# Kernel optimization log

Measured on AMD Instinct MI355X. Metric: run time of the kernel, lower is better.

The kernel has to match this reference:

```python
import jax, jax.numpy as jnp
import numpy as np

DIM = 2048
H = 16
QLR = 1536
KVLR = 512
NOPE = 128
ROPE = 64
VH = 128
QKH = NOPE + ROPE  # 192
B, S = 2, 2048
EPS = 1e-6


def _rmsnorm(x, w):
    return x * jax.lax.rsqrt(jnp.mean(x * x, axis=-1, keepdims=True) + EPS) * w


def _rope_cos_sin(seq_len, r, dtype):
    inv_freq = 1.0 / (10000.0 ** (jnp.arange(0, r, 2, dtype=jnp.float32) / r))
    ang = jnp.arange(seq_len, dtype=jnp.float32)[:, None] * inv_freq  # [S, r/2]
    return jnp.cos(ang).astype(dtype), jnp.sin(ang).astype(dtype)


def _rot(t, cos, sin):
    # rotate-half RoPE on last dim; cos/sin pre-broadcast to t's rank
    t1, t2 = jnp.split(t, 2, axis=-1)
    return jnp.concatenate([t1 * cos - t2 * sin, t2 * cos + t1 * sin], axis=-1)


def setup_inputs() -> dict:
    key = jax.random.key(0)
    ks = jax.random.split(key, 12)
    sd = 0.02
    return {
        "x": jax.random.normal(ks[0], (B, S, DIM), jnp.float32),
        "wqd": jax.random.normal(ks[1], (DIM, QLR), jnp.float32) * sd,
        "bqd": jnp.zeros((QLR,), jnp.float32),
        "qnorm_w": jnp.ones((QLR,), jnp.float32),
        "wqu": jax.random.normal(ks[2], (QLR, H * QKH), jnp.float32) * sd,
        "bqu": jnp.zeros((H * QKH,), jnp.float32),
        "wkvd": jax.random.normal(ks[3], (DIM, KVLR + ROPE), jnp.float32) * sd,
        "bkvd": jnp.zeros((KVLR + ROPE,), jnp.float32),
        "kvnorm_w": jnp.ones((KVLR,), jnp.float32),
        "wkvu": jax.random.normal(ks[4], (KVLR, H * (NOPE + VH)), jnp.float32) * sd,
        "bkvu": jnp.zeros((H * (NOPE + VH),), jnp.float32),
        "wout": jax.random.normal(ks[5], (H * VH, DIM), jnp.float32) * sd,
        "bout": jnp.zeros((DIM,), jnp.float32),
    }


def reference(x, wqd, bqd, qnorm_w, wqu, bqu, wkvd, bkvd, kvnorm_w, wkvu, bkvu, wout, bout):
    b, s, _ = x.shape
    # Q path: low-rank down, RMSNorm, up; split nope / rope
    q = _rmsnorm(x @ wqd + bqd, qnorm_w) @ wqu + bqu        # [b,s,H*QKH]
    q = q.reshape(b, s, H, QKH)
    q_nope, q_rope = q[..., :NOPE], q[..., NOPE:]
    # KV path: joint down-proj -> kv latent + shared rope key
    kvd = x @ wkvd + bkvd                                   # [b,s,KVLR+ROPE]
    kv_lora, k_rope = kvd[..., :KVLR], kvd[..., KVLR:]
    cos, sin = _rope_cos_sin(s, ROPE, x.dtype)
    q_rope = _rot(q_rope, cos[None, :, None, :], sin[None, :, None, :])
    k_rope = _rot(k_rope, cos[None, :, :], sin[None, :, :])  # [b,s,ROPE]
    kvu = _rmsnorm(kv_lora, kvnorm_w) @ wkvu + bkvu          # [b,s,H*(NOPE+VH)]
    kvu = kvu.reshape(b, s, H, NOPE + VH)
    k_nope, v = kvu[..., :NOPE], kvu[..., NOPE:]
    k_rope_b = jnp.broadcast_to(k_rope[:, :, None, :], (b, s, H, ROPE))
    qf = jnp.concatenate([q_nope, q_rope], axis=-1)          # [b,s,H,QKH]
    kf = jnp.concatenate([k_nope, k_rope_b], axis=-1)        # [b,s,H,QKH]
    scale = QKH ** -0.5
    scores = jnp.einsum('bqhd,bkhd->bhqk', qf, kf) * scale
    causal = jnp.tril(jnp.ones((s, s), bool))
    scores = jnp.where(causal, scores, jnp.finfo(scores.dtype).min)
    attn = jax.nn.softmax(scores, axis=-1)
    o = jnp.einsum('bhqk,bkhd->bqhd', attn, v).reshape(b, s, H * VH)
    return o @ wout + bout
```

## Files before the change

### kernel.cpp

```cpp
#include <hip/hip_runtime.h>
#include <hip/hip_bf16.h>
#include <math.h>

#define HH 16
#define SS 2048
#define BBATCH 2
#define NROWS 4096

typedef __attribute__((ext_vector_type(8))) __bf16 bf16x8;
typedef __attribute__((ext_vector_type(4))) float f32x4;
typedef const __attribute__((address_space(1))) unsigned int* gas1_t;
typedef __attribute__((address_space(3))) unsigned int* las3_t;

__device__ __forceinline__ unsigned short f2bf(float f) {
  unsigned u = __builtin_bit_cast(unsigned, f);
  u += 0x7fffu + ((u >> 16) & 1u);
  return (unsigned short)(u >> 16);
}
__device__ __forceinline__ float bf2f(unsigned short u) {
  return __builtin_bit_cast(float, (unsigned)u << 16);
}

__device__ __forceinline__ void gload16(const void* g, void* l) {
  __builtin_amdgcn_global_load_lds((gas1_t)g, (las3_t)l, 16, 0, 0);
}
__device__ __forceinline__ f32x4 mfma16(bf16x8 a, bf16x8 b, f32x4 c) {
  return __builtin_amdgcn_mfma_f32_16x16x32_bf16(a, b, c, 0, 0, 0);
}

__device__ __forceinline__ void transpose_body(const float* __restrict__ W,
                                               unsigned short* __restrict__ Wt,
                                               int K, int N, int Npad,
                                               int bx, int by, float (*tile)[33], int tid) {
  int n0 = bx * 32, k0 = by * 32;
  int tx = tid & 31, ty = tid >> 5;
  for (int i = ty; i < 32; i += 8) {
    int k = k0 + i, n = n0 + tx;
    tile[i][tx] = (k < K && n < N) ? W[(long)k * N + n] : 0.f;
  }
  __syncthreads();
  for (int i = ty; i < 32; i += 8) {
    int n = n0 + i, k = k0 + tx;
    if (n < Npad && k < K) Wt[(long)n * K + k] = f2bf(tile[tx][i]);
  }
}

__global__ __launch_bounds__(256) void k_prep(const float* __restrict__ x,
                                              unsigned short* __restrict__ xb,
                                              const float* __restrict__ wqd,
                                              const float* __restrict__ wqu,
                                              const float* __restrict__ wkvd,
                                              const float* __restrict__ wkvu,
                                              const float* __restrict__ wout,
                                              unsigned short* __restrict__ wqkt,
                                              unsigned short* __restrict__ wqut,
                                              unsigned short* __restrict__ wkvut,
                                              unsigned short* __restrict__ woutt,
                                              const float* __restrict__ bqd,
                                              const float* __restrict__ bkvd,
                                              float* __restrict__ mbias,
                                              float2* __restrict__ rtab) {
  __shared__ float tile[32][33];
  int blk = blockIdx.x;
  int tid = threadIdx.x;
  if (blk < 2048) {
    long n4 = (long)NROWS * 2048 / 4;
    for (long i = (long)blk * 256 + tid; i < n4; i += 2048 * 256) {
      float4 v = ((const float4*)x)[i];
      ushort4 o = { f2bf(v.x), f2bf(v.y), f2bf(v.z), f2bf(v.w) };
      ((ushort4*)xb)[i] = o;
    }
  } else if (blk < 5120) {
    int t = blk - 2048;
    transpose_body(wqd, wqkt, 2048, 1536, 1536, t % 48, t / 48, tile, tid);
  } else if (blk < 9728) {
    int t = blk - 5120;
    transpose_body(wqu, wqut, 1536, 3072, 3072, t % 96, t / 96, tile, tid);
  } else if (blk < 11008) {
    int t = blk - 9728;
    transpose_body(wkvd, wqkt + (size_t)1536 * 2048, 2048, 576, 640, t % 20, t / 20, tile, tid);
  } else if (blk < 13056) {
    int t = blk - 11008;
    transpose_body(wkvu, wkvut, 512, 4096, 4096, t % 128, t / 128, tile, tid);
  } else if (blk < 17152) {
    int t = blk - 13056;
    transpose_body(wout, woutt, 2048, 2048, 2048, t % 64, t / 64, tile, tid);
  } else if (blk < 17161) {
    int i = (blk - 17152) * 256 + tid;
    if (i < 2176) mbias[i] = i < 1536 ? bqd[i] : (i < 2112 ? bkvd[i - 1536] : 0.f);
  } else {
    int t = blk - 17161;
    int s = t * 8 + (tid >> 5);
    int i = tid & 31;
    float inv = powf(10000.f, -(float)i / 32.f);
    float ang = (float)s * inv;
    float sn, cs;
    sincosf(ang, &sn, &cs);
    rtab[s * 32 + i] = make_float2(cs, sn);
  }
}

__global__ __launch_bounds__(256) void k_gemm(const unsigned short* __restrict__ A,
                                              const unsigned short* __restrict__ Bt,
                                              const float* __restrict__ bias,
                                              float* __restrict__ C,
                                              int M, int N, int K) {
  __shared__ unsigned short lA[128 * 32];
  __shared__ unsigned short lB[128 * 32];
  int tid = threadIdx.x;
  int wave = tid >> 6, lane = tid & 63;
  int l15 = lane & 15, lhi = lane >> 4;
  int ntn = (N + 127) >> 7;
  int tm = blockIdx.x / ntn, tn = blockIdx.x % ntn;
  long row0 = (long)tm * 128, col0 = (long)tn * 128;
  int wr = wave >> 1, wc = wave & 1;

  const unsigned short* gA = A + (row0 + (tid >> 2)) * K + (tid & 3) * 8;
  const unsigned short* gB = Bt + (col0 + (tid >> 2)) * K + (tid & 3) * 8;
  unsigned short* lA0 = &lA[tid * 8];
  unsigned short* lB0 = &lB[tid * 8];

  f32x4 acc[4][4] = {};
  for (int k0 = 0; k0 < K; k0 += 32) {
    __syncthreads();
    gload16(gA + k0, lA0);
    gload16(gA + (long)64 * K + k0, lA0 + 2048);
    gload16(gB + k0, lB0);
    gload16(gB + (long)64 * K + k0, lB0 + 2048);
    asm volatile("s_waitcnt vmcnt(0)" ::: "memory");
    __syncthreads();
    bf16x8 af[4], bfr[4];
#pragma unroll
    for (int i = 0; i < 4; ++i) {
      af[i]  = *(const bf16x8*)&lA[(wr * 64 + i * 16 + l15) * 32 + lhi * 8];
      bfr[i] = *(const bf16x8*)&lB[(wc * 64 + i * 16 + l15) * 32 + lhi * 8];
    }
#pragma unroll
    for (int i = 0; i < 4; ++i)
#pragma unroll
      for (int j = 0; j < 4; ++j)
        acc[i][j] = mfma16(af[i], bfr[j], acc[i][j]);
  }
#pragma unroll
  for (int i = 0; i < 4; ++i)
#pragma unroll
    for (int j = 0; j < 4; ++j) {
      long r = row0 + wr * 64 + i * 16 + lhi * 4;
      long c = col0 + wc * 64 + j * 16 + l15;
      if (c < N) {
        float bv = bias[c];
#pragma unroll
        for (int rr = 0; rr < 4; ++rr)
          C[(r + rr) * N + c] = acc[i][j][rr] + bv;
      }
    }
}

__global__ __launch_bounds__(256) void k_gemm_c16(const unsigned short* __restrict__ A,
                                                  const unsigned short* __restrict__ Bt,
                                                  const float* __restrict__ bias,
                                                  unsigned short* __restrict__ C,
                                                  int M, int N, int K) {
  __shared__ unsigned short lA[128 * 32];
  __shared__ unsigned short lB[128 * 32];
  int tid = threadIdx.x;
  int wave = tid >> 6, lane = tid & 63;
  int l15 = lane & 15, lhi = lane >> 4;
  int ntn = (N + 127) >> 7;
  int tm = blockIdx.x / ntn, tn = blockIdx.x % ntn;
  long row0 = (long)tm * 128, col0 = (long)tn * 128;
  int wr = wave >> 1, wc = wave & 1;

  const unsigned short* gA = A + (row0 + (tid >> 2)) * K + (tid & 3) * 8;
  const unsigned short* gB = Bt + (col0 + (tid >> 2)) * K + (tid & 3) * 8;
  unsigned short* lA0 = &lA[tid * 8];
  unsigned short* lB0 = &lB[tid * 8];

  f32x4 acc[4][4] = {};
  for (int k0 = 0; k0 < K; k0 += 32) {
    __syncthreads();
    gload16(gA + k0, lA0);
    gload16(gA + (long)64 * K + k0, lA0 + 2048);
    gload16(gB + k0, lB0);
    gload16(gB + (long)64 * K + k0, lB0 + 2048);
    asm volatile("s_waitcnt vmcnt(0)" ::: "memory");
    __syncthreads();
    bf16x8 af[4], bfr[4];
#pragma unroll
    for (int i = 0; i < 4; ++i) {
      af[i]  = *(const bf16x8*)&lA[(wr * 64 + i * 16 + l15) * 32 + lhi * 8];
      bfr[i] = *(const bf16x8*)&lB[(wc * 64 + i * 16 + l15) * 32 + lhi * 8];
    }
#pragma unroll
    for (int i = 0; i < 4; ++i)
#pragma unroll
      for (int j = 0; j < 4; ++j)
        acc[i][j] = mfma16(af[i], bfr[j], acc[i][j]);
  }
#pragma unroll
  for (int i = 0; i < 4; ++i)
#pragma unroll
    for (int j = 0; j < 4; ++j) {
      long r = row0 + wr * 64 + i * 16 + lhi * 4;
      long c = col0 + wc * 64 + j * 16 + l15;
      if (c < N) {
        float bv = bias[c];
#pragma unroll
        for (int rr = 0; rr < 4; ++rr)
          C[(r + rr) * N + c] = f2bf(acc[i][j][rr] + bv);
      }
    }
}

__global__ __launch_bounds__(256) void k_gemm_qf(const unsigned short* __restrict__ A,
                                                 const unsigned short* __restrict__ Bt,
                                                 const float* __restrict__ bias,
                                                 const float2* __restrict__ rtab,
                                                 unsigned short* __restrict__ qf,
                                                 int M, int N, int K) {
  __shared__ unsigned short lA[128 * 32];
  __shared__ unsigned short lB[128 * 32];
  int tid = threadIdx.x;
  int wave = tid >> 6, lane = tid & 63;
  int l15 = lane & 15, lhi = lane >> 4;
  int ntn = (N + 127) >> 7;
  int tm = blockIdx.x / ntn, tn = blockIdx.x % ntn;
  long row0 = (long)tm * 128, col0 = (long)tn * 128;
  int wr = wave >> 1, wc = wave & 1;

  const unsigned short* gA = A + (row0 + (tid >> 2)) * K + (tid & 3) * 8;
  const unsigned short* gB = Bt + (col0 + (tid >> 2)) * K + (tid & 3) * 8;
  unsigned short* lA0 = &lA[tid * 8];
  unsigned short* lB0 = &lB[tid * 8];

  f32x4 acc[4][4] = {};
  for (int k0 = 0; k0 < K; k0 += 32) {
    __syncthreads();
    gload16(gA + k0, lA0);
    gload16(gA + (long)64 * K + k0, lA0 + 2048);
    gload16(gB + k0, lB0);
    gload16(gB + (long)64 * K + k0, lB0 + 2048);
    asm volatile("s_waitcnt vmcnt(0)" ::: "memory");
    __syncthreads();
    bf16x8 af[4], bfr[4];
#pragma unroll
    for (int i = 0; i < 4; ++i) {
      af[i]  = *(const bf16x8*)&lA[(wr * 64 + i * 16 + l15) * 32 + lhi * 8];
      bfr[i] = *(const bf16x8*)&lB[(wc * 64 + i * 16 + l15) * 32 + lhi * 8];
    }
#pragma unroll
    for (int i = 0; i < 4; ++i)
#pragma unroll
      for (int j = 0; j < 4; ++j)
        acc[i][j] = mfma16(af[i], bfr[j], acc[i][j]);
  }

  const float scq = 0.07216878364870322f * 1.4426950408889634f;
  int base = (int)col0 + wc * 64;
  int h = base / 192;
  int m192 = base - h * 192;
  float bv[4];
#pragma unroll
  for (int j = 0; j < 4; ++j) bv[j] = bias[base + j * 16 + l15];

#pragma unroll
  for (int i = 0; i < 4; ++i) {
#pragma unroll
    for (int rr = 0; rr < 4; ++rr) {
      long r = row0 + wr * 64 + i * 16 + lhi * 4 + rr;
      int s = (int)(r & 2047), b = (int)(r >> 11);
      unsigned short* dst = qf + (((long)(b * HH + h)) * SS + s) * 192;
      if (m192 < 128) {
#pragma unroll
        for (int j = 0; j < 4; ++j)
          dst[m192 + j * 16 + l15] = f2bf((acc[i][j][rr] + bv[j]) * scq);
      } else {
#pragma unroll
        for (int j = 0; j < 2; ++j) {
          int ifq = j * 16 + l15;
          float2 cs = rtab[s * 32 + ifq];
          float v1 = acc[i][j][rr] + bv[j];
          float v2 = acc[i][j + 2][rr] + bv[j + 2];
          dst[128 + ifq] = f2bf((v1 * cs.x - v2 * cs.y) * scq);
          dst[160 + ifq] = f2bf((v2 * cs.x + v1 * cs.y) * scq);
        }
      }
    }
  }
}

__global__ __launch_bounds__(256) void k_gemm_kv(const unsigned short* __restrict__ A,
                                                 const unsigned short* __restrict__ Bt,
                                                 const float* __restrict__ bias,
                                                 unsigned short* __restrict__ kf3,
                                                 unsigned short* __restrict__ vt3,
                                                 int M, int N, int K) {
  __shared__ unsigned short smem[16384];
  unsigned short* lA = smem;
  unsigned short* lB = smem + 4096;
  int tid = threadIdx.x;
  int wave = tid >> 6, lane = tid & 63;
  int l15 = lane & 15, lhi = lane >> 4;
  int ntn = N >> 7;
  int tm = blockIdx.x / ntn, tn = blockIdx.x % ntn;
  long row0 = (long)tm * 128, col0 = (long)tn * 128;
  int wr = wave >> 1, wc = wave & 1;

  const unsigned short* gA = A + (row0 + (tid >> 2)) * K + (tid & 3) * 8;
  const unsigned short* gB = Bt + (col0 + (tid >> 2)) * K + (tid & 3) * 8;
  unsigned short* lA0 = &lA[tid * 8];
  unsigned short* lB0 = &lB[tid * 8];

  f32x4 acc[4][4] = {};
  for (int k0 = 0; k0 < K; k0 += 32) {
    __syncthreads();
    gload16(gA + k0, lA0);
    gload16(gA + (long)64 * K + k0, lA0 + 2048);
    gload16(gB + k0, lB0);
    gload16(gB + (long)64 * K + k0, lB0 + 2048);
    asm volatile("s_waitcnt vmcnt(0)" ::: "memory");
    __syncthreads();
    bf16x8 af[4], bfr[4];
#pragma unroll
    for (int i = 0; i < 4; ++i) {
      af[i]  = *(const bf16x8*)&lA[(wr * 64 + i * 16 + l15) * 32 + lhi * 8];
      bfr[i] = *(const bf16x8*)&lB[(wc * 64 + i * 16 + l15) * 32 + lhi * 8];
    }
#pragma unroll
    for (int i = 0; i < 4; ++i)
#pragma unroll
      for (int j = 0; j < 4; ++j)
        acc[i][j] = mfma16(af[i], bfr[j], acc[i][j]);
  }

  int base = (int)col0 + wc * 64;
  int h = base >> 8;
  bool isv = (base & 255) >= 128;
  float bv[4];
#pragma unroll
  for (int j = 0; j < 4; ++j) bv[j] = bias[base + j * 16 + l15];

  int b = (int)(row0 >> 11);
  long bh = (long)b * HH + h;
  int lrb = wr * 64;
  __syncthreads();

  if (isv) {
#pragma unroll
    for (int i = 0; i < 4; ++i) {
      int lr = lrb + i * 16 + lhi * 4;
#pragma unroll
      for (int j = 0; j < 4; ++j) {
        int lc = wc * 64 + j * 16 + l15;
        ushort4 pk = { f2bf(acc[i][j][0] + bv[j]), f2bf(acc[i][j][1] + bv[j]),
                       f2bf(acc[i][j][2] + bv[j]), f2bf(acc[i][j][3] + bv[j]) };
        *(ushort4*)&smem[((lr >> 5) << 12) + lc * 32 + (lr & 31)] = pk;
      }
    }
    __syncthreads();
    long dst0 = (bh * 64 + ((row0 & 2047) >> 5)) * 4096;
#pragma unroll
    for (int p = 0; p < 8; ++p) {
      int e = p * 256 + tid;
      *(uint4*)&vt3[dst0 + e * 8] = *(uint4*)&smem[e * 8];
    }
  } else {
#pragma unroll
    for (int i = 0; i < 4; ++i) {
      int lr0 = lrb + i * 16 + lhi * 4;
#pragma unroll
      for (int j = 0; j < 4; ++j) {
        int c = (base & 255) + j * 16 + l15;
        int tbase = ((lr0 >> 4) << 11) + ((c >> 5) << 9) + (((c >> 3) & 3) << 7) + (c & 7);
#pragma unroll
        for (int rr = 0; rr < 4; ++rr)
          smem[tbase + ((lr0 + rr) & 15) * 8] = f2bf(acc[i][j][rr] + bv[j]);
      }
    }
    __syncthreads();
    long kb3 = (bh * 128 + ((row0 & 2047) >> 4)) * 3072;
#pragma unroll
    for (int p = 0; p < 8; ++p) {
      int e = p * 256 + tid;
      int tile = e >> 6;
      int off = (e & 63) * 8;
      long dst = kb3 + ((long)(tile >> 2) * 6 + (tile & 3)) * 512 + off;
      *(uint4*)&kf3[dst] = *(uint4*)&smem[tile * 512 + off];
    }
  }
}

__global__ __launch_bounds__(256) void k_rmsnorm2(const unsigned short* __restrict__ sC,
                                                  const float* __restrict__ qnw,
                                                  const float* __restrict__ kvnw,
                                                  unsigned short* __restrict__ qn,
                                                  unsigned short* __restrict__ kvn) {
  int blk = blockIdx.x;
  long row;
  const unsigned short* x;
  const float* w;
  unsigned short* y;
  int L;
  if (blk < NROWS) {
    row = blk; x = sC + row * 2176; w = qnw; y = qn + row * 1536; L = 1536;
  } else {
    row = blk - NROWS; x = sC + row * 2176 + 1536; w = kvnw; y = kvn + row * 512; L = 512;
  }
  float ss = 0.f;
  int n4 = L >> 2;
  for (int i = threadIdx.x; i < n4; i += 256) {
    ushort4 v = ((const ushort4*)x)[i];
    float a = bf2f(v.x), bb = bf2f(v.y), c = bf2f(v.z), d = bf2f(v.w);
    ss += a * a + bb * bb + c * c + d * d;
  }
  for (int off = 32; off > 0; off >>= 1) ss += __shfl_xor(ss, off);
  __shared__ float sb[4];
  if ((threadIdx.x & 63) == 0) sb[threadIdx.x >> 6] = ss;
  __syncthreads();
  float scale = rsqrtf((sb[0] + sb[1] + sb[2] + sb[3]) / (float)L + 1e-6f);
  for (int i = threadIdx.x; i < L; i += 256)
    y[i] = f2bf(bf2f(x[i]) * scale * w[i]);
}

__global__ __launch_bounds__(64) void k_extract_krope(const unsigned short* __restrict__ sC,
                                                      const float2* __restrict__ rtab,
                                                      unsigned short* __restrict__ kf3) {
  int bs = blockIdx.x;
  int lane = threadIdx.x;
  int s = bs & (SS - 1), b = bs >> 11;
  const unsigned short* src = sC + (long)bs * 2176 + 2048;
  int i = lane & 31;
  float2 cs = rtab[s * 32 + i];
  float t1 = bf2f(src[i]), t2 = bf2f(src[32 + i]);
  float v = (lane < 32) ? (t1 * cs.x - t2 * cs.y) : (t2 * cs.x + t1 * cs.y);
  unsigned short bv = f2bf(v);
  int d = 128 + lane;
  long inner = (long)(d >> 5) * 512 + ((d >> 3) & 3) * 128 + (s & 15) * 8 + (d & 7);
#pragma unroll
  for (int h = 0; h < HH; ++h) {
    long blk = ((long)(b * HH + h) * 128 + (s >> 4)) * 6;
    kf3[blk * 512 + inner] = bv;
  }
}

__global__ __launch_bounds__(256, 4) void k_attn(const unsigned short* __restrict__ qf,
                                                 const unsigned short* __restrict__ kf3,
                                                 const unsigned short* __restrict__ vt3,
                                                 unsigned short* __restrict__ o,
                                                 float* __restrict__ pO,
                                                 float* __restrict__ pml) {
  __shared__ unsigned short kbuf[64 * 192];
  __shared__ unsigned short pbuf[4][16 * 72];
  int tid = threadIdx.x;
  int wave = tid >> 6, lane = tid & 63;
  int l15 = lane & 15, lhi = lane >> 4;
  int idx = blockIdx.x;
  int rp = idx >> 5, bh = idx & 31;
  int qt, part, np;
  if (rp < 32)      { qt = 24 + (rp >> 2); part = rp & 3; np = 4; }
  else if (rp < 56) { int r = rp - 32; qt = 16 + r / 3; part = r % 3; np = 3; }
  else if (rp < 72) { int r = rp - 56; qt = 8 + (r >> 1); part = r & 1; np = 2; }
  else              { qt = 79 - rp; part = 0; np = 1; }
  int nt = qt + 1;
  int t0 = nt * part / np, t1 = nt * (part + 1) / np;
  bool dodiag = (part == np - 1);
  int item;
  if (np == 1) item = -1;
  else {
    int base = (qt < 16) ? (qt - 8) * 2 : (qt < 24) ? 16 + (qt - 16) * 3 : 40 + (qt - 24) * 4;
    item = bh * 72 + base + part;
  }
  int b = bh >> 4, h = bh & 15;
  int q0 = qt * 64;
  const char* kbase = (const char*)(kf3 + (long)bh * 128 * 3072);
  const unsigned short* vfrag0 = vt3 + (long)bh * 64 * 4096 + l15 * 32 + lhi * 8;
  const unsigned short* kread = kbuf + lane * 8;
  unsigned psel = 0x07060302u;

  {
    const char* src = kbase + (long)t0 * 24576 + tid * 16;
    char* dst = (char*)kbuf + tid * 16;
#pragma unroll
    for (int p = 0; p < 6; ++p) gload16(src + p * 4096, dst + p * 4096);
  }

  const unsigned short* Qb = qf + ((long)bh * SS + q0 + wave * 16 + l15) * 192 + lhi * 8;
  bf16x8 qfr[6];
#pragma unroll
  for (int ks = 0; ks < 6; ++ks) qfr[ks] = *(const bf16x8*)(Qb + ks * 32);

  float m = -3e38f, ls = 0.f;
  f32x4 acc[8] = {};
  int qin = wave * 16 + l15;

  for (int t = t0; t < t1; ++t) {
    asm volatile("s_waitcnt vmcnt(0)" ::: "memory");
    __builtin_amdgcn_s_barrier();
    __builtin_amdgcn_sched_barrier(0);

    f32x4 sc[4] = {};
    __builtin_amdgcn_s_setprio(1);
#pragma unroll
    for (int ks = 0; ks < 6; ++ks) {
      bf16x8 kfr[4];
#pragma unroll
      for (int nf = 0; nf < 4; ++nf)
        kfr[nf] = *(const bf16x8*)&kread[(nf * 6 + ks) * 512];
#pragma unroll
      for (int nf = 0; nf < 4; ++nf)
        sc[nf] = mfma16(kfr[nf], qfr[ks], sc[nf]);
    }
    __builtin_amdgcn_s_setprio(0);
    __builtin_amdgcn_sched_barrier(0);
    __builtin_amdgcn_s_barrier();
    __builtin_amdgcn_sched_barrier(0);

    const unsigned short* vtb = vfrag0 + (long)t * 8192;
    bf16x8 v0[8];
#pragma unroll
    for (int nf = 0; nf < 8; ++nf) v0[nf] = *(const bf16x8*)(vtb + nf * 512);
    __builtin_amdgcn_sched_barrier(0);

    if (t + 1 < t1) {
      const char* src = kbase + (long)(t + 1) * 24576 + tid * 16;
      char* dst = (char*)kbuf + tid * 16;
#pragma unroll
      for (int p = 0; p < 6; ++p) gload16(src + p * 4096, dst + p * 4096);
    }

    bool diag = dodiag && (t == t1 - 1);
    float mnf[4];
#pragma unroll
    for (int nf = 0; nf < 4; ++nf) {
      if (diag) {
#pragma unroll
        for (int jj = 0; jj < 4; ++jj) {
          int kin = nf * 16 + lhi * 4 + jj;
          if (kin > qin) sc[nf][jj] = -3e38f;
        }
      }
      mnf[nf] = fmaxf(fmaxf(sc[nf][0], sc[nf][1]), fmaxf(sc[nf][2], sc[nf][3]));
    }
    float mx = fmaxf(fmaxf(mnf[0], mnf[1]), fmaxf(mnf[2], mnf[3]));
    mx = fmaxf(mx, __shfl_xor(mx, 16));
    mx = fmaxf(mx, __shfl_xor(mx, 32));
    if (!__all(mx <= m + 8.f)) {
      float mn = fmaxf(m, mx);
      float alpha = exp2f(m - mn);
      m = mn;
      ls *= alpha;
#pragma unroll
      for (int nf = 0; nf < 8; ++nf)
#pragma unroll
        for (int jj = 0; jj < 4; ++jj) acc[nf][jj] *= alpha;
    }
    float pnf[4];
#pragma unroll
    for (int nf = 0; nf < 4; ++nf) {
      float e0 = exp2f(sc[nf][0] - m), e1 = exp2f(sc[nf][1] - m);
      float e2 = exp2f(sc[nf][2] - m), e3 = exp2f(sc[nf][3] - m);
      pnf[nf] = (e0 + e1) + (e2 + e3);
      unsigned lo, hi;
      asm("v_perm_b32 %0, %1, %2, %3" : "=v"(lo) : "v"(e1), "v"(e0), "s"(psel));
      asm("v_perm_b32 %0, %1, %2, %3" : "=v"(hi) : "v"(e3), "v"(e2), "s"(psel));
      uint2 pk = { lo, hi };
      *(uint2*)&pbuf[wave][l15 * 72 + nf * 16 + lhi * 4] = pk;
    }
    float ps = (pnf[0] + pnf[1]) + (pnf[2] + pnf[3]);
    ps += __shfl_xor(ps, 16);
    ps += __shfl_xor(ps, 32);
    ls += ps;

    {
      bf16x8 pf = *(const bf16x8*)&pbuf[wave][l15 * 72 + lhi * 8];
      __builtin_amdgcn_s_setprio(1);
#pragma unroll
      for (int nf = 0; nf < 8; ++nf) acc[nf] = mfma16(v0[nf], pf, acc[nf]);
      __builtin_amdgcn_s_setprio(0);
    }
    bf16x8 v1[8];
#pragma unroll
    for (int nf = 0; nf < 8; ++nf) v1[nf] = *(const bf16x8*)(vtb + 4096 + nf * 512);
    {
      bf16x8 pf = *(const bf16x8*)&pbuf[wave][l15 * 72 + 32 + lhi * 8];
      __builtin_amdgcn_s_setprio(1);
#pragma unroll
      for (int nf = 0; nf < 8; ++nf) acc[nf] = mfma16(v1[nf], pf, acc[nf]);
      __builtin_amdgcn_s_setprio(0);
    }
  }

  int qloc = wave * 16 + l15;
  if (item < 0) {
    float invl = 1.f / ls;
    long orow = (long)b * SS + q0 + qloc;
#pragma unroll
    for (int nf = 0; nf < 8; ++nf) {
      ushort4 ov = { f2bf(acc[nf][0] * invl), f2bf(acc[nf][1] * invl),
                     f2bf(acc[nf][2] * invl), f2bf(acc[nf][3] * invl) };
      *(ushort4*)&o[orow * 2048 + h * 128 + nf * 16 + lhi * 4] = ov;
    }
  } else {
    float* po = pO + (long)item * 8192 + qloc * 128;
#pragma unroll
    for (int nf = 0; nf < 8; ++nf)
      *(float4*)&po[nf * 16 + lhi * 4] = __builtin_bit_cast(float4, acc[nf]);
    if (lhi == 0) {
      pml[(long)item * 128 + qloc * 2] = m;
      pml[(long)item * 128 + qloc * 2 + 1] = ls;
    }
  }
}

__global__ __launch_bounds__(256) void k_merge(const float* __restrict__ pO,
                                               const float* __restrict__ pml,
                                               unsigned short* __restrict__ o) {
  int g = blockIdx.x;
  int bh = g / 24, qt = (g % 24) + 8;
  int b = bh >> 4, h = bh & 15;
  int q0 = qt * 64;
  int np = qt < 16 ? 2 : (qt < 24 ? 3 : 4);
  int base = (qt < 16) ? (qt - 8) * 2 : (qt < 24) ? 16 + (qt - 16) * 3 : 40 + (qt - 24) * 4;
  long i0 = (long)bh * 72 + base;
  __shared__ float wts[4][64];
  int tid = threadIdx.x;
  if (tid < 64) {
    float mp0 = -3e38f, mp1 = -3e38f, mp2 = -3e38f, mp3 = -3e38f;
    float lp0 = 0.f, lp1 = 0.f, lp2 = 0.f, lp3 = 0.f;
    mp0 = pml[(i0 + 0) * 128 + tid * 2]; lp0 = pml[(i0 + 0) * 128 + tid * 2 + 1];
    mp1 = pml[(i0 + 1) * 128 + tid * 2]; lp1 = pml[(i0 + 1) * 128 + tid * 2 + 1];
    if (np > 2) { mp2 = pml[(i0 + 2) * 128 + tid * 2]; lp2 = pml[(i0 + 2) * 128 + tid * 2 + 1]; }
    if (np > 3) { mp3 = pml[(i0 + 3) * 128 + tid * 2]; lp3 = pml[(i0 + 3) * 128 + tid * 2 + 1]; }
    float mm = fmaxf(fmaxf(mp0, mp1), fmaxf(mp2, mp3));
    float w0 = exp2f(mp0 - mm), w1 = exp2f(mp1 - mm);
    float w2 = (np > 2) ? exp2f(mp2 - mm) : 0.f;
    float w3 = (np > 3) ? exp2f(mp3 - mm) : 0.f;
    float inv = 1.f / (lp0 * w0 + lp1 * w1 + lp2 * w2 + lp3 * w3);
    wts[0][tid] = w0 * inv; wts[1][tid] = w1 * inv;
    wts[2][tid] = w2 * inv; wts[3][tid] = w3 * inv;
  }
  __syncthreads();
#pragma unroll
  for (int pp = 0; pp < 8; ++pp) {
    int e = pp * 256 + tid;
    int q = e >> 5, d4 = (e & 31) * 4;
    float4 s = { 0.f, 0.f, 0.f, 0.f };
#pragma unroll
    for (int p = 0; p < 4; ++p) {
      if (p < np) {
        float4 a = *(const float4*)&pO[(i0 + p) * 8192 + q * 128 + d4];
        float w = wts[p][q];
        s.x += a.x * w; s.y += a.y * w; s.z += a.z * w; s.w += a.w * w;
      }
    }
    ushort4 ov = { f2bf(s.x), f2bf(s.y), f2bf(s.z), f2bf(s.w) };
    *(ushort4*)&o[((long)b * SS + q0 + q) * 2048 + h * 128 + d4] = ov;
  }
}

extern "C" void kernel_launch(void* const* d_in, const int* in_sizes, int n_in,
                              void* d_out, int out_size, void* d_ws, size_t ws_size,
                              hipStream_t stream) {
  const float* x    = (const float*)d_in[0];
  const float* wqd  = (const float*)d_in[1];
  const float* bqd  = (const float*)d_in[2];
  const float* qnw  = (const float*)d_in[3];
  const float* wqu  = (const float*)d_in[4];
  const float* bqu  = (const float*)d_in[5];
  const float* wkvd = (const float*)d_in[6];
  const float* bkvd = (const float*)d_in[7];
  const float* kvnw = (const float*)d_in[8];
  const float* wkvu = (const float*)d_in[9];
  const float* bkvu = (const float*)d_in[10];
  const float* wout = (const float*)d_in[11];
  const float* bout = (const float*)d_in[12];
  float* out = (float*)d_out;

  char* ws = (char*)d_ws;
  size_t off = 0;
  auto alloc = [&](size_t sz) {
    char* p = ws + off;
    off += (sz + 255) & ~(size_t)255;
    return p;
  };
  unsigned short* xb    = (unsigned short*)alloc((size_t)NROWS * 2048 * 2);
  unsigned short* wqkt  = (unsigned short*)alloc((size_t)2176 * 2048 * 2);
  unsigned short* wqut  = (unsigned short*)alloc((size_t)3072 * 1536 * 2);
  unsigned short* wkvut = (unsigned short*)alloc((size_t)4096 * 512 * 2);
  unsigned short* woutt = (unsigned short*)alloc((size_t)2048 * 2048 * 2);
  unsigned short* qn    = (unsigned short*)alloc((size_t)NROWS * 1536 * 2);
  unsigned short* kvn   = (unsigned short*)alloc((size_t)NROWS * 512 * 2);
  unsigned short* qfb   = (unsigned short*)alloc((size_t)32 * SS * 192 * 2);
  unsigned short* kfb   = (unsigned short*)alloc((size_t)32 * SS * 192 * 2);
  unsigned short* vtb   = (unsigned short*)alloc((size_t)32 * 128 * SS * 2);
  unsigned short* ob    = (unsigned short*)alloc((size_t)NROWS * 2048 * 2);
  float*  mbias = (float*)alloc((size_t)2176 * 4);
  float2* rtab  = (float2*)alloc((size_t)SS * 32 * 8);
  float*  pO    = (float*)alloc((size_t)2304 * 8192 * 4);
  float*  pml   = (float*)alloc((size_t)2304 * 128 * 4);
  unsigned short* sCb = (unsigned short*)alloc((size_t)NROWS * 2176 * 2);

  k_prep<<<17417, 256, 0, stream>>>(x, xb, wqd, wqu, wkvd, wkvu, wout,
                                    wqkt, wqut, wkvut, woutt, bqd, bkvd, mbias, rtab);

  k_gemm_c16<<<32 * 17, 256, 0, stream>>>(xb, wqkt, mbias, sCb, NROWS, 2176, 2048);

  k_rmsnorm2<<<2 * NROWS, 256, 0, stream>>>(sCb, qnw, kvnw, qn, kvn);

  k_gemm_qf<<<32 * 24, 256, 0, stream>>>(qn, wqut, bqu, rtab, qfb, NROWS, 3072, 1536);

  k_extract_krope<<<NROWS, 64, 0, stream>>>(sCb, rtab, kfb);
  k_gemm_kv<<<32 * 32, 256, 0, stream>>>(kvn, wkvut, bkvu, kfb, vtb, NROWS, 4096, 512);

  k_attn<<<2560, 256, 0, stream>>>(qfb, kfb, vtb, ob, pO, pml);
  k_merge<<<768, 256, 0, stream>>>(pO, pml, ob);

  k_gemm<<<32 * 16, 256, 0, stream>>>(ob, woutt, bout, out, NROWS, 2048, 2048);
}
```

Baseline: 400.4 us.

## Merge Q/KV up-projection and k-rope kernels into one launch; swizzle attn P buffer

```diff
diff --git a/kernel.cpp b/kernel.cpp
--- a/kernel.cpp
+++ b/kernel.cpp
@@ -212,180 +212,185 @@
     }
 }
 
-__global__ __launch_bounds__(256) void k_gemm_qf(const unsigned short* __restrict__ A,
-                                                 const unsigned short* __restrict__ Bt,
-                                                 const float* __restrict__ bias,
-                                                 const float2* __restrict__ rtab,
-                                                 unsigned short* __restrict__ qf,
-                                                 int M, int N, int K) {
-  __shared__ unsigned short lA[128 * 32];
-  __shared__ unsigned short lB[128 * 32];
+__global__ __launch_bounds__(256) void k_up(const unsigned short* __restrict__ qn,
+                                            const unsigned short* __restrict__ wqut,
+                                            const float* __restrict__ bqu,
+                                            const unsigned short* __restrict__ kvn,
+                                            const unsigned short* __restrict__ wkvut,
+                                            const float* __restrict__ bkvu,
+                                            const unsigned short* __restrict__ sCb,
+                                            const float2* __restrict__ rtab,
+                                            unsigned short* __restrict__ qf,
+                                            unsigned short* __restrict__ kf3,
+                                            unsigned short* __restrict__ vt3) {
+  __shared__ unsigned short smem[16384];
+  unsigned short* lA = smem;
+  unsigned short* lB = smem + 4096;
+  int blk = blockIdx.x;
   int tid = threadIdx.x;
   int wave = tid >> 6, lane = tid & 63;
   int l15 = lane & 15, lhi = lane >> 4;
-  int ntn = (N + 127) >> 7;
-  int tm = blockIdx.x / ntn, tn = blockIdx.x % ntn;
-  long row0 = (long)tm * 128, col0 = (long)tn * 128;
   int wr = wave >> 1, wc = wave & 1;
 
-  const unsigned short* gA = A + (row0 + (tid >> 2)) * K + (tid & 3) * 8;
-  const unsigned short* gB = Bt + (col0 + (tid >> 2)) * K + (tid & 3) * 8;
-  unsigned short* lA0 = &lA[tid * 8];
-  unsigned short* lB0 = &lB[tid * 8];
-
-  f32x4 acc[4][4] = {};
-  for (int k0 = 0; k0 < K; k0 += 32) {
+  if (blk < 768) {
+    const int N = 3072, K = 1536;
+    int tm = blk / 24, tn = blk % 24;
+    long row0 = (long)tm * 128, col0 = (long)tn * 128;
+    const unsigned short* gA = qn + (row0 + (tid >> 2)) * K + (tid & 3) * 8;
+    const unsigned short* gB = wqut + (col0 + (tid >> 2)) * K + (tid & 3) * 8;
+    unsigned short* lA0 = &lA[tid * 8];
+    unsigned short* lB0 = &lB[tid * 8];
+    f32x4 acc[4][4] = {};
+    for (int k0 = 0; k0 < K; k0 += 32) {
+      __syncthreads();
+      gload16(gA + k0, lA0);
+      gload16(gA + (long)64 * K + k0, lA0 + 2048);
+      gload16(gB + k0, lB0);
+      gload16(gB + (long)64 * K + k0, lB0 + 2048);
+      asm volatile("s_waitcnt vmcnt(0)" ::: "memory");
+      __syncthreads();
+      bf16x8 af[4], bfr[4];
+#pragma unroll
+      for (int i = 0; i < 4; ++i) {
+        af[i]  = *(const bf16x8*)&lA[(wr * 64 + i * 16 + l15) * 32 + lhi * 8];
+        bfr[i] = *(const bf16x8*)&lB[(wc * 64 + i * 16 + l15) * 32 + lhi * 8];
+      }
+#pragma unroll
+      for (int i = 0; i < 4; ++i)
+#pragma unroll
+        for (int j = 0; j < 4; ++j)
+          acc[i][j] = mfma16(af[i], bfr[j], acc[i][j]);
+    }
+    const float scq = 0.07216878364870322f * 1.4426950408889634f;
+    int base = (int)col0 + wc * 64;
+    int h = base / 192;
+    int m192 = base - h * 192;
+    float bv[4];
+#pragma unroll
+    for (int j = 0; j < 4; ++j) bv[j] = bqu[base + j * 16 + l15];
+#pragma unroll
+    for (int i = 0; i < 4; ++i) {
+#pragma unroll
+      for (int rr = 0; rr < 4; ++rr) {
+        long r = row0 + wr * 64 + i * 16 + lhi * 4 + rr;
+        int s = (int)(r & 2047), b = (int)(r >> 11);
+        unsigned short* dst = qf + (((long)(b * HH + h)) * SS + s) * 192;
+        if (m192 < 128) {
+#pragma unroll
+          for (int j = 0; j < 4; ++j)
+            dst[m192 + j * 16 + l15] = f2bf((acc[i][j][rr] + bv[j]) * scq);
+        } else {
+#pragma unroll
+          for (int j = 0; j < 2; ++j) {
+            int ifq = j * 16 + l15;
+            float2 cs = rtab[s * 32 + ifq];
+            float v1 = acc[i][j][rr] + bv[j];
+            float v2 = acc[i][j + 2][rr] + bv[j + 2];
+            dst[128 + ifq] = f2bf((v1 * cs.x - v2 * cs.y) * scq);
+            dst[160 + ifq] = f2bf((v2 * cs.x + v1 * cs.y) * scq);
+          }
+        }
+      }
+    }
+  } else if (blk < 1792) {
+    const int N = 4096, K = 512;
+    int b2 = blk - 768;
+    int tm = b2 / 32, tn = b2 % 32;
+    long row0 = (long)tm * 128, col0 = (long)tn * 128;
+    const unsigned short* gA = kvn + (row0 + (tid >> 2)) * K + (tid & 3) * 8;
+    const unsigned short* gB = wkvut + (col0 + (tid >> 2)) * K + (tid & 3) * 8;
+    unsigned short* lA0 = &lA[tid * 8];
+    unsigned short* lB0 = &lB[tid * 8];
+    f32x4 acc[4][4] = {};
+    for (int k0 = 0; k0 < K; k0 += 32) {
+      __syncthreads();
+      gload16(gA + k0, lA0);
+      gload16(gA + (long)64 * K + k0, lA0 + 2048);
+      gload16(gB + k0, lB0);
+      gload16(gB + (long)64 * K + k0, lB0 + 2048);
+      asm volatile("s_waitcnt vmcnt(0)" ::: "memory");
+      __syncthreads();
+      bf16x8 af[4], bfr[4];
+#pragma unroll
+      for (int i = 0; i < 4; ++i) {
+        af[i]  = *(const bf16x8*)&lA[(wr * 64 + i * 16 + l15) * 32 + lhi * 8];
+        bfr[i] = *(const bf16x8*)&lB[(wc * 64 + i * 16 + l15) * 32 + lhi * 8];
+      }
+#pragma unroll
+      for (int i = 0; i < 4; ++i)
+#pragma unroll
+        for (int j = 0; j < 4; ++j)
+          acc[i][j] = mfma16(af[i], bfr[j], acc[i][j]);
+    }
+    int base = (int)col0 + wc * 64;
+    int h = base >> 8;
+    bool isv = (base & 255) >= 128;
+    float bv[4];
+#pragma unroll
+    for (int j = 0; j < 4; ++j) bv[j] = bkvu[base + j * 16 + l15];
+    int b = (int)(row0 >> 11);
+    long bh = (long)b * HH + h;
+    int lrb = wr * 64;
     __syncthreads();
-    gload16(gA + k0, lA0);
-    gload16(gA + (long)64 * K + k0, lA0 + 2048);
-    gload16(gB + k0, lB0);
-    gload16(gB + (long)64 * K + k0, lB0 + 2048);
-    asm volatile("s_waitcnt vmcnt(0)" ::: "memory");
-    __syncthreads();
-    bf16x8 af[4], bfr[4];
-#pragma unroll
-    for (int i = 0; i < 4; ++i) {
-      af[i]  = *(const bf16x8*)&lA[(wr * 64 + i * 16 + l15) * 32 + lhi * 8];
-      bfr[i] = *(const bf16x8*)&lB[(wc * 64 + i * 16 + l15) * 32 + lhi * 8];
-    }
-#pragma unroll
-    for (int i = 0; i < 4; ++i)
-#pragma unroll
-      for (int j = 0; j < 4; ++j)
-        acc[i][j] = mfma16(af[i], bfr[j], acc[i][j]);
-  }
-
-  const float scq = 0.07216878364870322f * 1.4426950408889634f;
-  int base = (int)col0 + wc * 64;
-  int h = base / 192;
-  int m192 = base - h * 192;
-  float bv[4];
-#pragma unroll
-  for (int j = 0; j < 4; ++j) bv[j] = bias[base + j * 16 + l15];
-
-#pragma unroll
-  for (int i = 0; i < 4; ++i) {
-#pragma unroll
-    for (int rr = 0; rr < 4; ++rr) {
-      long r = row0 + wr * 64 + i * 16 + lhi * 4 + rr;
-      int s = (int)(r & 2047), b = (int)(r >> 11);
-      unsigned short* dst = qf + (((long)(b * HH + h)) * SS + s) * 192;
-      if (m192 < 128) {
-#pragma unroll
-        for (int j = 0; j < 4; ++j)
-          dst[m192 + j * 16 + l15] = f2bf((acc[i][j][rr] + bv[j]) * scq);
-      } else {
-#pragma unroll
-        for (int j = 0; j < 2; ++j) {
-          int ifq = j * 16 + l15;
-          float2 cs = rtab[s * 32 + ifq];
-          float v1 = acc[i][j][rr] + bv[j];
-          float v2 = acc[i][j + 2][rr] + bv[j + 2];
-          dst[128 + ifq] = f2bf((v1 * cs.x - v2 * cs.y) * scq);
-          dst[160 + ifq] = f2bf((v2 * cs.x + v1 * cs.y) * scq);
+    if (isv) {
+#pragma unroll
+      for (int i = 0; i < 4; ++i) {
+        int lr = lrb + i * 16 + lhi * 4;
+#pragma unroll
+        for (int j = 0; j < 4; ++j) {
+          int lc = wc * 64 + j * 16 + l15;
+          ushort4 pk = { f2bf(acc[i][j][0] + bv[j]), f2bf(acc[i][j][1] + bv[j]),
+                         f2bf(acc[i][j][2] + bv[j]), f2bf(acc[i][j][3] + bv[j]) };
+          *(ushort4*)&smem[((lr >> 5) << 12) + lc * 32 + (lr & 31)] = pk;
         }
       }
-    }
-  }
-}
-
-__global__ __launch_bounds__(256) void k_gemm_kv(const unsigned short* __restrict__ A,
-                                                 const unsigned short* __restrict__ Bt,
-                                                 const float* __restrict__ bias,
-                                                 unsigned short* __restrict__ kf3,
-                                                 unsigned short* __restrict__ vt3,
-                                                 int M, int N, int K) {
-  __shared__ unsigned short smem[16384];
-  unsigned short* lA = smem;
-  unsigned short* lB = smem + 4096;
-  int tid = threadIdx.x;
-  int wave = tid >> 6, lane = tid & 63;
-  int l15 = lane & 15, lhi = lane >> 4;
-  int ntn = N >> 7;
-  int tm = blockIdx.x / ntn, tn = blockIdx.x % ntn;
-  long row0 = (long)tm * 128, col0 = (long)tn * 128;
-  int wr = wave >> 1, wc = wave & 1;
-
-  const unsigned short* gA = A + (row0 + (tid >> 2)) * K + (tid & 3) * 8;
-  const unsigned short* gB = Bt + (col0 + (tid >> 2)) * K + (tid & 3) * 8;
-  unsigned short* lA0 = &lA[tid * 8];
-  unsigned short* lB0 = &lB[tid * 8];
-
-  f32x4 acc[4][4] = {};
-  for (int k0 = 0; k0 < K; k0 += 32) {
-    __syncthreads();
-    gload16(gA + k0, lA0);
-    gload16(gA + (long)64 * K + k0, lA0 + 2048);
-    gload16(gB + k0, lB0);
-    gload16(gB + (long)64 * K + k0, lB0 + 2048);
-    asm volatile("s_waitcnt vmcnt(0)" ::: "memory");
-    __syncthreads();
-    bf16x8 af[4], bfr[4];
-#pragma unroll
-    for (int i = 0; i < 4; ++i) {
-      af[i]  = *(const bf16x8*)&lA[(wr * 64 + i * 16 + l15) * 32 + lhi * 8];
-      bfr[i] = *(const bf16x8*)&lB[(wc * 64 + i * 16 + l15) * 32 + lhi * 8];
-    }
-#pragma unroll
-    for (int i = 0; i < 4; ++i)
-#pragma unroll
-      for (int j = 0; j < 4; ++j)
-        acc[i][j] = mfma16(af[i], bfr[j], acc[i][j]);
-  }
-
-  int base = (int)col0 + wc * 64;
-  int h = base >> 8;
-  bool isv = (base & 255) >= 128;
-  float bv[4];
-#pragma unroll
-  for (int j = 0; j < 4; ++j) bv[j] = bias[base + j * 16 + l15];
-
-  int b = (int)(row0 >> 11);
-  long bh = (long)b * HH + h;
-  int lrb = wr * 64;
-  __syncthreads();
-
-  if (isv) {
-#pragma unroll
-    for (int i = 0; i < 4; ++i) {
-      int lr = lrb + i * 16 + lhi * 4;
-#pragma unroll
-      for (int j = 0; j < 4; ++j) {
-        int lc = wc * 64 + j * 16 + l15;
-        ushort4 pk = { f2bf(acc[i][j][0] + bv[j]), f2bf(acc[i][j][1] + bv[j]),
-                       f2bf(acc[i][j][2] + bv[j]), f2bf(acc[i][j][3] + bv[j]) };
-        *(ushort4*)&smem[((lr >> 5) << 12) + lc * 32 + (lr & 31)] = pk;
-      }
-    }
-    __syncthreads();
-    long dst0 = (bh * 64 + ((row0 & 2047) >> 5)) * 4096;
-#pragma unroll
-    for (int p = 0; p < 8; ++p) {
-      int e = p * 256 + tid;
-      *(uint4*)&vt3[dst0 + e * 8] = *(uint4*)&smem[e * 8];
+      __syncthreads();
+      long dst0 = (bh * 64 + ((row0 & 2047) >> 5)) * 4096;
+#pragma unroll
+      for (int p = 0; p < 8; ++p) {
+        int e = p * 256 + tid;
+        *(uint4*)&vt3[dst0 + e * 8] = *(uint4*)&smem[e * 8];
+      }
+    } else {
+#pragma unroll
+      for (int i = 0; i < 4; ++i) {
+        int lr0 = lrb + i * 16 + lhi * 4;
+#pragma unroll
+        for (int j = 0; j < 4; ++j) {
+          int c = (base & 255) + j * 16 + l15;
+          int tbase = ((lr0 >> 4) << 11) + ((c >> 5) << 9) + (((c >> 3) & 3) << 7) + (c & 7);
+#pragma unroll
+          for (int rr = 0; rr < 4; ++rr)
+            smem[tbase + ((lr0 + rr) & 15) * 8] = f2bf(acc[i][j][rr] + bv[j]);
+        }
+      }
+      __syncthreads();
+      long kb3 = (bh * 128 + ((row0 & 2047) >> 4)) * 3072;
+#pragma unroll
+      for (int p = 0; p < 8; ++p) {
+        int e = p * 256 + tid;
+        int tile = e >> 6;
+        int off = (e & 63) * 8;
+        long dst = kb3 + ((long)(tile >> 2) * 6 + (tile & 3)) * 512 + off;
+        *(uint4*)&kf3[dst] = *(uint4*)&smem[tile * 512 + off];
+      }
     }
   } else {
-#pragma unroll
-    for (int i = 0; i < 4; ++i) {
-      int lr0 = lrb + i * 16 + lhi * 4;
-#pragma unroll
-      for (int j = 0; j < 4; ++j) {
-        int c = (base & 255) + j * 16 + l15;
-        int tbase = ((lr0 >> 4) << 11) + ((c >> 5) << 9) + (((c >> 3) & 3) << 7) + (c & 7);
-#pragma unroll
-        for (int rr = 0; rr < 4; ++rr)
-          smem[tbase + ((lr0 + rr) & 15) * 8] = f2bf(acc[i][j][rr] + bv[j]);
-      }
-    }
-    __syncthreads();
-    long kb3 = (bh * 128 + ((row0 & 2047) >> 4)) * 3072;
-#pragma unroll
-    for (int p = 0; p < 8; ++p) {
-      int e = p * 256 + tid;
-      int tile = e >> 6;
-      int off = (e & 63) * 8;
-      long dst = kb3 + ((long)(tile >> 2) * 6 + (tile & 3)) * 512 + off;
-      *(uint4*)&kf3[dst] = *(uint4*)&smem[tile * 512 + off];
+    int t = blk - 1792;
+    int bs = t * 4 + (tid >> 6);
+    int s = bs & (SS - 1), b = bs >> 11;
+    const unsigned short* src = sCb + (long)bs * 2176 + 2048;
+    int i = lane & 31;
+    float2 cs = rtab[s * 32 + i];
+    float t1 = bf2f(src[i]), t2 = bf2f(src[32 + i]);
+    float v = (lane < 32) ? (t1 * cs.x - t2 * cs.y) : (t2 * cs.x + t1 * cs.y);
+    unsigned short bv = f2bf(v);
+    int d = 128 + lane;
+    long inner = (long)(d >> 5) * 512 + ((d >> 3) & 3) * 128 + (s & 15) * 8 + (d & 7);
+#pragma unroll
+    for (int h = 0; h < HH; ++h) {
+      long kblk = ((long)(b * HH + h) * 128 + (s >> 4)) * 6;
+      kf3[kblk * 512 + inner] = bv;
     }
   }
 }
@@ -422,35 +427,14 @@
     y[i] = f2bf(bf2f(x[i]) * scale * w[i]);
 }
 
-__global__ __launch_bounds__(64) void k_extract_krope(const unsigned short* __restrict__ sC,
-                                                      const float2* __restrict__ rtab,
-                                                      unsigned short* __restrict__ kf3) {
-  int bs = blockIdx.x;
-  int lane = threadIdx.x;
-  int s = bs & (SS - 1), b = bs >> 11;
-  const unsigned short* src = sC + (long)bs * 2176 + 2048;
-  int i = lane & 31;
-  float2 cs = rtab[s * 32 + i];
-  float t1 = bf2f(src[i]), t2 = bf2f(src[32 + i]);
-  float v = (lane < 32) ? (t1 * cs.x - t2 * cs.y) : (t2 * cs.x + t1 * cs.y);
-  unsigned short bv = f2bf(v);
-  int d = 128 + lane;
-  long inner = (long)(d >> 5) * 512 + ((d >> 3) & 3) * 128 + (s & 15) * 8 + (d & 7);
-#pragma unroll
-  for (int h = 0; h < HH; ++h) {
-    long blk = ((long)(b * HH + h) * 128 + (s >> 4)) * 6;
-    kf3[blk * 512 + inner] = bv;
-  }
-}
-
-__global__ __launch_bounds__(256, 4) void k_attn(const unsigned short* __restrict__ qf,
+__global__ __launch_bounds__(256, 5) void k_attn(const unsigned short* __restrict__ qf,
                                                  const unsigned short* __restrict__ kf3,
                                                  const unsigned short* __restrict__ vt3,
                                                  unsigned short* __restrict__ o,
                                                  float* __restrict__ pO,
                                                  float* __restrict__ pml) {
   __shared__ unsigned short kbuf[64 * 192];
-  __shared__ unsigned short pbuf[4][16 * 72];
+  __shared__ unsigned short pbuf[4][16 * 64];
   int tid = threadIdx.x;
   int wave = tid >> 6, lane = tid & 63;
   int l15 = lane & 15, lhi = lane >> 4;
@@ -476,6 +460,7 @@
   const unsigned short* vfrag0 = vt3 + (long)bh * 64 * 4096 + l15 * 32 + lhi * 8;
   const unsigned short* kread = kbuf + lane * 8;
   unsigned psel = 0x07060302u;
+  int pswz = (l15 & 7) << 3;
 
   {
     const char* src = kbase + (long)t0 * 24576 + tid * 16;
@@ -564,7 +549,7 @@
       asm("v_perm_b32 %0, %1, %2, %3" : "=v"(lo) : "v"(e1), "v"(e0), "s"(psel));
       asm("v_perm_b32 %0, %1, %2, %3" : "=v"(hi) : "v"(e3), "v"(e2), "s"(psel));
       uint2 pk = { lo, hi };
-      *(uint2*)&pbuf[wave][l15 * 72 + nf * 16 + lhi * 4] = pk;
+      *(uint2*)&pbuf[wave][l15 * 64 + ((nf * 16 + lhi * 4) ^ pswz)] = pk;
     }
     float ps = (pnf[0] + pnf[1]) + (pnf[2] + pnf[3]);
     ps += __shfl_xor(ps, 16);
@@ -572,7 +557,7 @@
     ls += ps;
 
     {
-      bf16x8 pf = *(const bf16x8*)&pbuf[wave][l15 * 72 + lhi * 8];
+      bf16x8 pf = *(const bf16x8*)&pbuf[wave][l15 * 64 + ((lhi * 8) ^ pswz)];
       __builtin_amdgcn_s_setprio(1);
 #pragma unroll
       for (int nf = 0; nf < 8; ++nf) acc[nf] = mfma16(v0[nf], pf, acc[nf]);
@@ -582,7 +567,7 @@
 #pragma unroll
     for (int nf = 0; nf < 8; ++nf) v1[nf] = *(const bf16x8*)(vtb + 4096 + nf * 512);
     {
-      bf16x8 pf = *(const bf16x8*)&pbuf[wave][l15 * 72 + 32 + lhi * 8];
+      bf16x8 pf = *(const bf16x8*)&pbuf[wave][l15 * 64 + ((32 + lhi * 8) ^ pswz)];
       __builtin_amdgcn_s_setprio(1);
 #pragma unroll
       for (int nf = 0; nf < 8; ++nf) acc[nf] = mfma16(v1[nf], pf, acc[nf]);
@@ -707,10 +692,8 @@
 
   k_rmsnorm2<<<2 * NROWS, 256, 0, stream>>>(sCb, qnw, kvnw, qn, kvn);
 
-  k_gemm_qf<<<32 * 24, 256, 0, stream>>>(qn, wqut, bqu, rtab, qfb, NROWS, 3072, 1536);
-
-  k_extract_krope<<<NROWS, 64, 0, stream>>>(sCb, rtab, kfb);
-  k_gemm_kv<<<32 * 32, 256, 0, stream>>>(kvn, wkvut, bkvu, kfb, vtb, NROWS, 4096, 512);
+  k_up<<<2816, 256, 0, stream>>>(qn, wqut, bqu, kvn, wkvut, bkvu, sCb, rtab,
+                                 qfb, kfb, vtb);
 
   k_attn<<<2560, 256, 0, stream>>>(qfb, kfb, vtb, ob, pO, pml);
   k_merge<<<768, 256, 0, stream>>>(pO, pml, ob);
```

After: 609.2 us. +52.2%, slower.
